# Optimization experiments

Hardware: AMD Instinct MI355X
Metric: run time of the kernel (lower is better)

Reference implementation:

```python
import jax, jax.numpy as jnp
import numpy as np

B, T, C = 4, 2048, 1024
N_HEAD = 16
HEAD_DIM = C // N_HEAD


def setup_inputs() -> dict:
    key = jax.random.key(0)
    k1, k2, k3 = jax.random.split(key, 3)
    x = jax.random.normal(k1, (B, T, C), dtype=jnp.float32)
    W_attn = jax.random.normal(k2, (C, 3 * C), dtype=jnp.float32) * (1.0 / np.sqrt(C))
    b_attn = jnp.zeros((3 * C,), dtype=jnp.float32)
    W_proj = jax.random.normal(k3, (C, C), dtype=jnp.float32) * (1.0 / np.sqrt(C))
    b_proj = jnp.zeros((C,), dtype=jnp.float32)
    return {"x": x, "W_attn": W_attn, "b_attn": b_attn, "W_proj": W_proj, "b_proj": b_proj}


def reference(x, W_attn, b_attn, W_proj, b_proj):
    Bx, Tx, Cx = x.shape
    qkv = x @ W_attn + b_attn  # (B,T,3C)
    q, k, v = jnp.split(qkv, 3, axis=-1)
    # (B, n_head, T, head_dim)
    def to_heads(t):
        return t.reshape(Bx, Tx, N_HEAD, HEAD_DIM).transpose(0, 2, 1, 3)
    q, k, v = to_heads(q), to_heads(k), to_heads(v)
    scale = 1.0 / np.sqrt(HEAD_DIM)
    scores = jnp.einsum('bhqd,bhkd->bhqk', q, k) * scale  # (B,H,T,T)
    causal = jnp.tril(jnp.ones((Tx, Tx), dtype=bool))
    scores = jnp.where(causal[None, None, :, :], scores, -jnp.inf)
    probs = jax.nn.softmax(scores, axis=-1)
    attn = jnp.einsum('bhqk,bhkd->bhqd', probs, v)  # (B,H,T,D)
    attn = attn.transpose(0, 2, 1, 3).reshape(Bx, Tx, Cx)
    return attn @ W_proj + b_proj
```

## Files before the change

kernel.cpp:

```cpp
#include <hip/hip_runtime.h>


typedef __attribute__((ext_vector_type(8))) __bf16 bf16x8;
typedef __attribute__((ext_vector_type(4))) float f32x4;
typedef __attribute__((ext_vector_type(4))) short s16x4;

__device__ __forceinline__ float bf2f(unsigned short h) {
    unsigned u = ((unsigned)h) << 16;
    return __builtin_bit_cast(float, u);
}
__device__ __forceinline__ unsigned short f2bf(float f) {
    unsigned u = __builtin_bit_cast(unsigned, f);
    u += 0x7fffu + ((u >> 16) & 1u);
    return (unsigned short)(u >> 16);
}
__device__ __forceinline__ unsigned pack2bf(float a, float b) {
    return (unsigned)f2bf(a) | ((unsigned)f2bf(b) << 16);
}
__device__ __forceinline__ void gload16(const unsigned short* g, unsigned short* l) {
    __builtin_amdgcn_global_load_lds(
        (const __attribute__((address_space(1))) unsigned int*)g,
        (__attribute__((address_space(3))) unsigned int*)l, 16, 0, 0);
}

__global__ void convert_kernel(const float* __restrict__ in, unsigned short* __restrict__ out,
                               long n) {
    long i = ((long)blockIdx.x * blockDim.x + threadIdx.x) * 4;
    if (i >= n) return;
    f32x4 v = *reinterpret_cast<const f32x4*>(&in[i]);
    s16x4 o;
    o[0] = (short)f2bf(v[0]);
    o[1] = (short)f2bf(v[1]);
    o[2] = (short)f2bf(v[2]);
    o[3] = (short)f2bf(v[3]);
    *reinterpret_cast<s16x4*>(&out[i]) = o;
}

__global__ void transpose_kernel(const float* __restrict__ W,
                                 unsigned short* __restrict__ Wt,
                                 int K, int N) {
    __shared__ float t[32][33];
    const int tid = threadIdx.x;
    const int n0 = blockIdx.x * 32, k0 = blockIdx.y * 32;
    const int row = tid >> 3, c4 = (tid & 7) * 4;
    f32x4 v = *reinterpret_cast<const f32x4*>(&W[(size_t)(k0 + row) * N + n0 + c4]);
    t[row][c4 + 0] = v[0];
    t[row][c4 + 1] = v[1];
    t[row][c4 + 2] = v[2];
    t[row][c4 + 3] = v[3];
    __syncthreads();
    s16x4 o;
    o[0] = (short)f2bf(t[c4 + 0][row]);
    o[1] = (short)f2bf(t[c4 + 1][row]);
    o[2] = (short)f2bf(t[c4 + 2][row]);
    o[3] = (short)f2bf(t[c4 + 3][row]);
    *reinterpret_cast<s16x4*>(&Wt[(size_t)(n0 + row) * K + k0 + c4]) = o;
}

template <int MODE>
__global__ __launch_bounds__(256, 2)
void gemm_kernel(const unsigned short* __restrict__ A,
                 const unsigned short* __restrict__ Bt,
                 const float* __restrict__ bias,
                 float* __restrict__ Cout,
                 unsigned short* __restrict__ Qo,
                 unsigned short* __restrict__ Ko,
                 unsigned short* __restrict__ Vto,
                 int M, int N, int Kd) {
    __shared__ unsigned short As[2][128 * 32];
    __shared__ unsigned short Bs[2][128 * 32];
    const int tid = threadIdx.x;
    const int wave = tid >> 6, lane = tid & 63;
    const int l15 = lane & 15, lhi = lane >> 4;
    const int wm = wave >> 1, wn = wave & 1;
    const int m0 = blockIdx.x * 128, n0 = blockIdx.y * 128;

    f32x4 acc[4][4];
#pragma unroll
    for (int i = 0; i < 4; i++)
#pragma unroll
        for (int j = 0; j < 4; j++) acc[i][j] = f32x4{0.f, 0.f, 0.f, 0.f};

    const int r0 = tid >> 2, cb = (tid & 3) * 8;
    const unsigned short* Ap = &A[(size_t)(m0 + r0) * Kd + cb];
    const unsigned short* Bp = &Bt[(size_t)(n0 + r0) * Kd + cb];
    const size_t K64 = (size_t)64 * Kd;

#define STAGE(buf, k0)                                      \
    do {                                                    \
        gload16(Ap + (k0), &As[buf][tid * 8]);              \
        gload16(Ap + K64 + (k0), &As[buf][64 * 32 + tid * 8]); \
        gload16(Bp + (k0), &Bs[buf][tid * 8]);              \
        gload16(Bp + K64 + (k0), &Bs[buf][64 * 32 + tid * 8]); \
    } while (0)

#define COMPUTE(buf)                                                                         \
    do {                                                                                     \
        bf16x8 af[4], bfr[4];                                                                \
        _Pragma("unroll") for (int i = 0; i < 4; i++) {                                      \
            af[i]  = *reinterpret_cast<const bf16x8*>(&As[buf][(wm * 64 + i * 16 + l15) * 32 + lhi * 8]); \
            bfr[i] = *reinterpret_cast<const bf16x8*>(&Bs[buf][(wn * 64 + i * 16 + l15) * 32 + lhi * 8]); \
        }                                                                                    \
        _Pragma("unroll") for (int i = 0; i < 4; i++)                                        \
            _Pragma("unroll") for (int j = 0; j < 4; j++)                                    \
                acc[i][j] = __builtin_amdgcn_mfma_f32_16x16x32_bf16(af[i], bfr[j], acc[i][j], 0, 0, 0); \
    } while (0)

    STAGE(0, 0);
    __syncthreads();
    for (int k0 = 0; k0 < Kd; k0 += 64) {
        STAGE(1, k0 + 32);
        COMPUTE(0);
        __syncthreads();
        if (k0 + 64 < Kd) STAGE(0, k0 + 64);
        COMPUTE(1);
        __syncthreads();
    }
#undef STAGE
#undef COMPUTE

#pragma unroll
    for (int j = 0; j < 4; j++) {
        const int col = n0 + wn * 64 + j * 16 + l15;
        const float bv = bias[col];
#pragma unroll
        for (int i = 0; i < 4; i++) {
            const int rbase = m0 + wm * 64 + i * 16 + lhi * 4;
#pragma unroll
            for (int r = 0; r < 4; r++) {
                const int row = rbase + r;
                const float oval = acc[i][j][r] + bv;
                if (MODE == 0) {
                    Cout[(size_t)row * N + col] = oval;
                } else {
                    const int sel = col >> 10, c1 = col & 1023;
                    const int h = c1 >> 6, d = c1 & 63;
                    const int b = row >> 11, t = row & 2047;
                    if (sel == 0)
                        Qo[(((size_t)(b * 16 + h)) * 2048 + t) * 64 + d] = f2bf(oval * 0.125f);
                    else if (sel == 1)
                        Ko[(((size_t)(b * 16 + h)) * 2048 + t) * 64 + d] = f2bf(oval);
                    else
                        Vto[(((size_t)(b * 16 + h)) * 64 + d) * 2048 + t] = f2bf(oval);
                }
            }
        }
    }
}

__global__ __launch_bounds__(256, 2)
void attn_kernel(const unsigned short* __restrict__ Q,
                 const unsigned short* __restrict__ Kg,
                 const unsigned short* __restrict__ Vt,
                 unsigned short* __restrict__ Aout) {
    __shared__ unsigned int Pl[4][16 * 36];
    const int tid = threadIdx.x, wave = tid >> 6, lane = tid & 63;
    const int l15 = lane & 15, lhi = lane >> 4;
    const int bid = blockIdx.x;
    const int head = bid & 63;
    const int j = bid >> 6;
    const int qb = (j < 4) ? j : (11 - j);
    const int q0w = qb * 256 + wave * 64;
    const unsigned short* Qh = Q + (size_t)head * (2048 * 64);
    const unsigned short* Kh = Kg + (size_t)head * (2048 * 64);
    const unsigned short* Vh = Vt + (size_t)head * (64 * 2048);
    unsigned int* P = &Pl[wave][0];

    bf16x8 qfr[4][2];
#pragma unroll
    for (int qf = 0; qf < 4; qf++)
#pragma unroll
        for (int dh = 0; dh < 2; dh++)
            qfr[qf][dh] = *reinterpret_cast<const bf16x8*>(
                &Qh[(size_t)(q0w + qf * 16 + l15) * 64 + dh * 32 + lhi * 8]);

    f32x4 o[4][4];
#pragma unroll
    for (int df = 0; df < 4; df++)
#pragma unroll
        for (int qf = 0; qf < 4; qf++) o[df][qf] = f32x4{0.f, 0.f, 0.f, 0.f};
    float m[4] = {-1e30f, -1e30f, -1e30f, -1e30f};
    float l[4] = {0.f, 0.f, 0.f, 0.f};

    const int ntiles = (q0w >> 6) + 1;
    for (int t = 0; t < ntiles; ++t) {
        const int kt = t * 64;
        const bool masked = (t == ntiles - 1);
        bf16x8 kfr[4][2], vfr[4][2];
#pragma unroll
        for (int kf = 0; kf < 4; kf++)
#pragma unroll
            for (int dh = 0; dh < 2; dh++)
                kfr[kf][dh] = *reinterpret_cast<const bf16x8*>(
                    &Kh[(size_t)(kt + kf * 16 + l15) * 64 + dh * 32 + lhi * 8]);
#pragma unroll
        for (int df = 0; df < 4; df++)
#pragma unroll
            for (int kc = 0; kc < 2; kc++)
                vfr[df][kc] = *reinterpret_cast<const bf16x8*>(
                    &Vh[(size_t)(df * 16 + l15) * 2048 + kt + kc * 32 + lhi * 8]);

#pragma unroll
        for (int qf = 0; qf < 4; qf++) {
            f32x4 s[4];
#pragma unroll
            for (int kf = 0; kf < 4; kf++) {
                s[kf] = __builtin_amdgcn_mfma_f32_16x16x32_bf16(kfr[kf][0], qfr[qf][0],
                                                                f32x4{0.f, 0.f, 0.f, 0.f}, 0, 0, 0);
                s[kf] = __builtin_amdgcn_mfma_f32_16x16x32_bf16(kfr[kf][1], qfr[qf][1], s[kf], 0, 0, 0);
            }
            if (masked) {
#pragma unroll
                for (int kf = 0; kf < 4; kf++)
#pragma unroll
                    for (int r = 0; r < 4; r++)
                        if (kf * 16 + lhi * 4 + r > qf * 16 + l15) s[kf][r] = -1e30f;
            }
            float tm = s[0][0];
#pragma unroll
            for (int kf = 0; kf < 4; kf++)
#pragma unroll
                for (int r = 0; r < 4; r++) tm = fmaxf(tm, s[kf][r]);
            tm = fmaxf(tm, __shfl_xor(tm, 16));
            tm = fmaxf(tm, __shfl_xor(tm, 32));
            const float mn = fmaxf(m[qf], tm);
            const float corr = __expf(m[qf] - mn);
            m[qf] = mn;
            float rs = 0.f;
#pragma unroll
            for (int kf = 0; kf < 4; kf++)
#pragma unroll
                for (int r = 0; r < 4; r++) {
                    const float p = __expf(s[kf][r] - mn);
                    s[kf][r] = p;
                    rs += p;
                }
            rs += __shfl_xor(rs, 16);
            rs += __shfl_xor(rs, 32);
            l[qf] = l[qf] * corr + rs;
#pragma unroll
            for (int df = 0; df < 4; df++)
#pragma unroll
                for (int r = 0; r < 4; r++) o[df][qf][r] *= corr;

#pragma unroll
            for (int kf = 0; kf < 4; kf++) {
                P[l15 * 36 + kf * 8 + lhi * 2 + 0] = pack2bf(s[kf][0], s[kf][1]);
                P[l15 * 36 + kf * 8 + lhi * 2 + 1] = pack2bf(s[kf][2], s[kf][3]);
            }
            asm volatile("s_waitcnt lgkmcnt(0)" ::: "memory");
            bf16x8 pb0 = *reinterpret_cast<const bf16x8*>(&P[l15 * 36 + 0 * 16 + lhi * 4]);
            bf16x8 pb1 = *reinterpret_cast<const bf16x8*>(&P[l15 * 36 + 1 * 16 + lhi * 4]);
#pragma unroll
            for (int df = 0; df < 4; df++) {
                o[df][qf] = __builtin_amdgcn_mfma_f32_16x16x32_bf16(vfr[df][0], pb0, o[df][qf], 0, 0, 0);
                o[df][qf] = __builtin_amdgcn_mfma_f32_16x16x32_bf16(vfr[df][1], pb1, o[df][qf], 0, 0, 0);
            }
        }
    }

    const int b = head >> 4, h = head & 15;
#pragma unroll
    for (int qf = 0; qf < 4; qf++) {
        const float inv = 1.0f / l[qf];
        unsigned short* op = Aout + ((size_t)(b * 2048 + q0w + qf * 16 + l15)) * 1024 + h * 64;
#pragma unroll
        for (int df = 0; df < 4; df++) {
            *reinterpret_cast<unsigned*>(&op[df * 16 + lhi * 4]) =
                pack2bf(o[df][qf][0] * inv, o[df][qf][1] * inv);
            *reinterpret_cast<unsigned*>(&op[df * 16 + lhi * 4 + 2]) =
                pack2bf(o[df][qf][2] * inv, o[df][qf][3] * inv);
        }
    }
}

extern "C" void kernel_launch(void* const* d_in, const int* in_sizes, int n_in,
                              void* d_out, int out_size, void* d_ws, size_t ws_size,
                              hipStream_t stream) {
    const float* x     = (const float*)d_in[0];
    const float* Wattn = (const float*)d_in[1];
    const float* battn = (const float*)d_in[2];
    const float* Wproj = (const float*)d_in[3];
    const float* bproj = (const float*)d_in[4];
    float* out = (float*)d_out;

    unsigned short* ws = (unsigned short*)d_ws;
    const size_t HS = (size_t)4 * 16 * 2048 * 64;
    unsigned short* Qb  = ws;
    unsigned short* Kb  = Qb + HS;
    unsigned short* Vtb = Kb + HS;
    unsigned short* Ab  = Vtb + HS;
    unsigned short* Wta = Ab + HS;
    unsigned short* Wtp = Wta + (size_t)3072 * 1024;
    unsigned short* xb  = Wtp + (size_t)1024 * 1024;

    convert_kernel<<<8192, 256, 0, stream>>>(x, xb, (long)HS);
    transpose_kernel<<<dim3(96, 32), 256, 0, stream>>>(Wattn, Wta, 1024, 3072);
    transpose_kernel<<<dim3(32, 32), 256, 0, stream>>>(Wproj, Wtp, 1024, 1024);
    gemm_kernel<1><<<dim3(64, 24), 256, 0, stream>>>(xb, Wta, battn, nullptr, Qb, Kb, Vtb,
                                                     8192, 3072, 1024);
    attn_kernel<<<512, 256, 0, stream>>>(Qb, Kb, Vtb, Ab);
    gemm_kernel<0><<<dim3(64, 8), 256, 0, stream>>>(Ab, Wtp, bproj, out, nullptr, nullptr, nullptr,
                                                    8192, 1024, 1024);
}
```

Baseline: 218.6 us.

## Add 256x256-tile QKV GEMM with swizzled LDS, deeper pipeline and XCD-aware block mapping

Replaces the 128x128 QKV projection GEMM with a dedicated 512-thread kernel using 256x256 output tiles. It uses an XOR-swizzled LDS layout, a multi-stage global_load_lds pipeline with explicit vmcnt waits and barriers, and s_setprio around the MFMA bursts. Block indices are remapped so neighbouring tiles land on the same XCD for better L2 reuse. The larger tiles raise arithmetic intensity and cut LDS bank conflicts, at the cost of one block per CU, much higher register and LDS use, and only 384 blocks.

```diff
diff --git a/kernel.cpp b/kernel.cpp
--- a/kernel.cpp
+++ b/kernel.cpp
@@ -5,10 +5,6 @@
 typedef __attribute__((ext_vector_type(4))) float f32x4;
 typedef __attribute__((ext_vector_type(4))) short s16x4;
 
-__device__ __forceinline__ float bf2f(unsigned short h) {
-    unsigned u = ((unsigned)h) << 16;
-    return __builtin_bit_cast(float, u);
-}
 __device__ __forceinline__ unsigned short f2bf(float f) {
     unsigned u = __builtin_bit_cast(unsigned, f);
     u += 0x7fffu + ((u >> 16) & 1u);
@@ -57,15 +53,124 @@
     *reinterpret_cast<s16x4*>(&Wt[(size_t)(n0 + row) * K + k0 + c4]) = o;
 }
 
-template <int MODE>
+__global__ __launch_bounds__(512, 1)
+void gemm256_kernel(const unsigned short* __restrict__ A,
+                    const unsigned short* __restrict__ Bt,
+                    const float* __restrict__ bias,
+                    unsigned short* __restrict__ Qo,
+                    unsigned short* __restrict__ Ko,
+                    unsigned short* __restrict__ Vto,
+                    int Kd) {
+    __shared__ unsigned short As[2][2][256 * 32];
+    __shared__ unsigned short Bs[2][2][256 * 32];
+    const int tid = threadIdx.x;
+    const int wave = tid >> 6, lane = tid & 63;
+    const int l15 = lane & 15, lhi = lane >> 4;
+    const int wm = wave >> 2, wn = wave & 3;
+    const int sw = (l15 & 8) << 2;
+    const int wg = (blockIdx.x & 7) * 48 + (blockIdx.x >> 3);
+    const int bm = wg / 12, bn = wg % 12;
+    const int m0 = bm * 256, n0 = bn * 256;
+
+    f32x4 acc[8][4];
+#pragma unroll
+    for (int i = 0; i < 8; i++)
+#pragma unroll
+        for (int j = 0; j < 4; j++) acc[i][j] = f32x4{0.f, 0.f, 0.f, 0.f};
+
+    const int L0 = tid * 16;
+    const int Ls0 = L0 ^ (((L0 >> 9) & 1) << 5);
+    const size_t ga0 = (size_t)(Ls0 >> 6) * Kd + ((Ls0 & 63) >> 1);
+    const size_t ga1 = ga0 + (size_t)128 * Kd;
+    const unsigned short* Ap = A + (size_t)m0 * Kd;
+    const unsigned short* Bp = Bt + (size_t)n0 * Kd;
+
+#define STAGEH(dst, src, kofs)                                                    \
+    do {                                                                          \
+        gload16((src) + ga0 + (kofs), (unsigned short*)((char*)(dst) + L0));      \
+        gload16((src) + ga1 + (kofs), (unsigned short*)((char*)(dst) + 8192 + L0)); \
+    } while (0)
+
+#define VWAIT2 asm volatile("s_waitcnt vmcnt(2)" ::: "memory")
+
+#define PHASE(db, ks, qm, STMT, WAITS)                                                     \
+    do {                                                                                   \
+        char* ab_ = (char*)&As[db][ks][0];                                                 \
+        char* bb_ = (char*)&Bs[db][ks][0];                                                 \
+        const int ar_ = (wm * 128 + (qm) * 64 + l15) * 64 + (lhi * 16 ^ sw);               \
+        const int br_ = (wn * 64 + l15) * 64 + (lhi * 16 ^ sw);                            \
+        bf16x8 av_[4], bv_[4];                                                             \
+        _Pragma("unroll") for (int t_ = 0; t_ < 4; t_++) {                                 \
+            av_[t_] = *(const bf16x8*)(ab_ + ar_ + t_ * 1024);                             \
+            bv_[t_] = *(const bf16x8*)(bb_ + br_ + t_ * 1024);                             \
+        }                                                                                  \
+        STMT;                                                                              \
+        WAITS;                                                                             \
+        __builtin_amdgcn_s_barrier();                                                      \
+        __builtin_amdgcn_s_setprio(1);                                                     \
+        _Pragma("unroll") for (int t_ = 0; t_ < 4; t_++)                                   \
+            _Pragma("unroll") for (int n_ = 0; n_ < 4; n_++)                               \
+                acc[(qm) * 4 + t_][n_] = __builtin_amdgcn_mfma_f32_16x16x32_bf16(          \
+                    av_[t_], bv_[n_], acc[(qm) * 4 + t_][n_], 0, 0, 0);                    \
+        __builtin_amdgcn_s_setprio(0);                                                     \
+        __builtin_amdgcn_s_barrier();                                                      \
+    } while (0)
+
+    STAGEH(&As[0][0][0], Ap, 0);
+    STAGEH(&Bs[0][0][0], Bp, 0);
+    STAGEH(&As[0][1][0], Ap, 32);
+    STAGEH(&Bs[0][1][0], Bp, 32);
+    STAGEH(&As[1][0][0], Ap, 64);
+    VWAIT2;
+    __builtin_amdgcn_s_barrier();
+
+    const int NITER = Kd >> 7;
+    for (int i = 0; i < NITER; ++i) {
+        const int kt1 = (2 * i + 1) * 64, kt2 = (2 * i + 2) * 64, kt3 = kt2 + 64;
+        const bool sg = (i < NITER - 1);
+        PHASE(0, 0, 0, { STAGEH(&Bs[1][0][0], Bp, kt1); }, );
+        PHASE(0, 1, 0, { STAGEH(&As[1][1][0], Ap, kt1 + 32); }, );
+        PHASE(0, 0, 1, { STAGEH(&Bs[1][1][0], Bp, kt1 + 32); }, );
+        PHASE(0, 1, 1, { if (sg) STAGEH(&As[0][0][0], Ap, kt2); }, VWAIT2);
+        PHASE(1, 0, 0, { if (sg) STAGEH(&Bs[0][0][0], Bp, kt2); }, );
+        PHASE(1, 1, 0, { if (sg) STAGEH(&As[0][1][0], Ap, kt2 + 32); }, );
+        PHASE(1, 0, 1, { if (sg) STAGEH(&Bs[0][1][0], Bp, kt2 + 32); }, );
+        PHASE(1, 1, 1, { if (sg) STAGEH(&As[1][0][0], Ap, kt3); }, VWAIT2);
+    }
+#undef PHASE
+#undef STAGEH
+#undef VWAIT2
+
+#pragma unroll
+    for (int nf = 0; nf < 4; nf++) {
+        const int col = n0 + wn * 64 + nf * 16 + l15;
+        const float bv = bias[col];
+        const int sel = col >> 10, c1 = col & 1023;
+        const int h = c1 >> 6, d = c1 & 63;
+#pragma unroll
+        for (int mf = 0; mf < 8; mf++) {
+            const int rbase = m0 + wm * 128 + mf * 16 + lhi * 4;
+#pragma unroll
+            for (int r = 0; r < 4; r++) {
+                const int row = rbase + r;
+                const float oval = acc[mf][nf][r] + bv;
+                const int b = row >> 11, t = row & 2047;
+                if (sel == 0)
+                    Qo[(((size_t)(b * 16 + h)) * 2048 + t) * 64 + d] = f2bf(oval * 0.125f);
+                else if (sel == 1)
+                    Ko[(((size_t)(b * 16 + h)) * 2048 + t) * 64 + d] = f2bf(oval);
+                else
+                    Vto[(((size_t)(b * 16 + h)) * 64 + d) * 2048 + t] = f2bf(oval);
+            }
+        }
+    }
+}
+
 __global__ __launch_bounds__(256, 2)
 void gemm_kernel(const unsigned short* __restrict__ A,
                  const unsigned short* __restrict__ Bt,
                  const float* __restrict__ bias,
                  float* __restrict__ Cout,
-                 unsigned short* __restrict__ Qo,
-                 unsigned short* __restrict__ Ko,
-                 unsigned short* __restrict__ Vto,
                  int M, int N, int Kd) {
     __shared__ unsigned short As[2][128 * 32];
     __shared__ unsigned short Bs[2][128 * 32];
@@ -86,11 +191,11 @@
     const unsigned short* Bp = &Bt[(size_t)(n0 + r0) * Kd + cb];
     const size_t K64 = (size_t)64 * Kd;
 
-#define STAGE(buf, k0)                                      \
-    do {                                                    \
-        gload16(Ap + (k0), &As[buf][tid * 8]);              \
+#define STAGE(buf, k0)                                         \
+    do {                                                       \
+        gload16(Ap + (k0), &As[buf][tid * 8]);                 \
         gload16(Ap + K64 + (k0), &As[buf][64 * 32 + tid * 8]); \
-        gload16(Bp + (k0), &Bs[buf][tid * 8]);              \
+        gload16(Bp + (k0), &Bs[buf][tid * 8]);                 \
         gload16(Bp + K64 + (k0), &Bs[buf][64 * 32 + tid * 8]); \
     } while (0)
 
@@ -127,23 +232,8 @@
         for (int i = 0; i < 4; i++) {
             const int rbase = m0 + wm * 64 + i * 16 + lhi * 4;
 #pragma unroll
-            for (int r = 0; r < 4; r++) {
-                const int row = rbase + r;
-                const float oval = acc[i][j][r] + bv;
-                if (MODE == 0) {
-                    Cout[(size_t)row * N + col] = oval;
-                } else {
-                    const int sel = col >> 10, c1 = col & 1023;
-                    const int h = c1 >> 6, d = c1 & 63;
-                    const int b = row >> 11, t = row & 2047;
-                    if (sel == 0)
-                        Qo[(((size_t)(b * 16 + h)) * 2048 + t) * 64 + d] = f2bf(oval * 0.125f);
-                    else if (sel == 1)
-                        Ko[(((size_t)(b * 16 + h)) * 2048 + t) * 64 + d] = f2bf(oval);
-                    else
-                        Vto[(((size_t)(b * 16 + h)) * 64 + d) * 2048 + t] = f2bf(oval);
-                }
-            }
+            for (int r = 0; r < 4; r++)
+                Cout[(size_t)(rbase + r) * N + col] = acc[i][j][r] + bv;
         }
     }
 }
@@ -297,9 +387,7 @@
     convert_kernel<<<8192, 256, 0, stream>>>(x, xb, (long)HS);
     transpose_kernel<<<dim3(96, 32), 256, 0, stream>>>(Wattn, Wta, 1024, 3072);
     transpose_kernel<<<dim3(32, 32), 256, 0, stream>>>(Wproj, Wtp, 1024, 1024);
-    gemm_kernel<1><<<dim3(64, 24), 256, 0, stream>>>(xb, Wta, battn, nullptr, Qb, Kb, Vtb,
-                                                     8192, 3072, 1024);
+    gemm256_kernel<<<384, 512, 0, stream>>>(xb, Wta, battn, Qb, Kb, Vtb, 1024);
     attn_kernel<<<512, 256, 0, stream>>>(Qb, Kb, Vtb, Ab);
-    gemm_kernel<0><<<dim3(64, 8), 256, 0, stream>>>(Ab, Wtp, bproj, out, nullptr, nullptr, nullptr,
-                                                    8192, 1024, 1024);
-}
+    gemm_kernel<<<dim3(64, 8), 256, 0, stream>>>(Ab, Wtp, bproj, out, 8192, 1024, 1024);
+}
```

Result: slower. 244.7 us (+11.9%).

## Deepen GEMM LDS pipeline to four stages with swizzled layout and manual waitcnt

Applied to the files above, without the earlier changes.

The GEMM mainloop moves from a double-buffered LDS scheme with __syncthreads to a four-slot ring that prefetches two k-steps ahead. It uses explicit vmcnt waits, raw s_barrier and s_setprio around the MFMA block. An XOR swizzle on the k-column offset is applied to both the global-to-LDS staging and the fragment reads, to cut LDS bank conflicts. This doubles LDS usage per block, which may reduce occupancy, and correctness now depends on hand-counted vmcnt values and on Kd being a multiple of 128.

```diff
diff --git a/kernel.cpp b/kernel.cpp
--- a/kernel.cpp
+++ b/kernel.cpp
@@ -5,10 +5,6 @@
 typedef __attribute__((ext_vector_type(4))) float f32x4;
 typedef __attribute__((ext_vector_type(4))) short s16x4;
 
-__device__ __forceinline__ float bf2f(unsigned short h) {
-    unsigned u = ((unsigned)h) << 16;
-    return __builtin_bit_cast(float, u);
-}
 __device__ __forceinline__ unsigned short f2bf(float f) {
     unsigned u = __builtin_bit_cast(unsigned, f);
     u += 0x7fffu + ((u >> 16) & 1u);
@@ -67,8 +63,8 @@
                  unsigned short* __restrict__ Ko,
                  unsigned short* __restrict__ Vto,
                  int M, int N, int Kd) {
-    __shared__ unsigned short As[2][128 * 32];
-    __shared__ unsigned short Bs[2][128 * 32];
+    __shared__ unsigned short As[4][128 * 32];
+    __shared__ unsigned short Bs[4][128 * 32];
     const int tid = threadIdx.x;
     const int wave = tid >> 6, lane = tid & 63;
     const int l15 = lane & 15, lhi = lane >> 4;
@@ -81,43 +77,66 @@
 #pragma unroll
         for (int j = 0; j < 4; j++) acc[i][j] = f32x4{0.f, 0.f, 0.f, 0.f};
 
-    const int r0 = tid >> 2, cb = (tid & 3) * 8;
-    const unsigned short* Ap = &A[(size_t)(m0 + r0) * Kd + cb];
-    const unsigned short* Bp = &Bt[(size_t)(n0 + r0) * Kd + cb];
+    const int r0 = tid >> 2;
+    const int cstage = (((tid & 3) ^ (r0 & 3)) << 3);
+    const unsigned short* Ap = &A[(size_t)(m0 + r0) * Kd + cstage];
+    const unsigned short* Bp = &Bt[(size_t)(n0 + r0) * Kd + cstage];
     const size_t K64 = (size_t)64 * Kd;
-
-#define STAGE(buf, k0)                                      \
-    do {                                                    \
-        gload16(Ap + (k0), &As[buf][tid * 8]);              \
-        gload16(Ap + K64 + (k0), &As[buf][64 * 32 + tid * 8]); \
-        gload16(Bp + (k0), &Bs[buf][tid * 8]);              \
-        gload16(Bp + K64 + (k0), &Bs[buf][64 * 32 + tid * 8]); \
+    const int csw = (lhi * 8) ^ ((l15 & 3) << 3);
+
+#define STAGE(sl, k0)                                   \
+    do {                                                \
+        gload16(Ap + (k0), &As[sl][tid * 8]);           \
+        gload16(Ap + K64 + (k0), &As[sl][2048 + tid * 8]); \
+        gload16(Bp + (k0), &Bs[sl][tid * 8]);           \
+        gload16(Bp + K64 + (k0), &Bs[sl][2048 + tid * 8]); \
     } while (0)
 
-#define COMPUTE(buf)                                                                         \
-    do {                                                                                     \
-        bf16x8 af[4], bfr[4];                                                                \
-        _Pragma("unroll") for (int i = 0; i < 4; i++) {                                      \
-            af[i]  = *reinterpret_cast<const bf16x8*>(&As[buf][(wm * 64 + i * 16 + l15) * 32 + lhi * 8]); \
-            bfr[i] = *reinterpret_cast<const bf16x8*>(&Bs[buf][(wn * 64 + i * 16 + l15) * 32 + lhi * 8]); \
-        }                                                                                    \
-        _Pragma("unroll") for (int i = 0; i < 4; i++)                                        \
-            _Pragma("unroll") for (int j = 0; j < 4; j++)                                    \
-                acc[i][j] = __builtin_amdgcn_mfma_f32_16x16x32_bf16(af[i], bfr[j], acc[i][j], 0, 0, 0); \
+#define VW4 asm volatile("s_waitcnt vmcnt(4)" ::: "memory")
+#define VW0 asm volatile("s_waitcnt vmcnt(0)" ::: "memory")
+
+#define PH(sl, sg, kc, WAITM)                                                              \
+    do {                                                                                   \
+        bf16x8 av_[4], bv_[4];                                                             \
+        _Pragma("unroll") for (int i_ = 0; i_ < 4; i_++) {                                 \
+            av_[i_] = *reinterpret_cast<const bf16x8*>(                                    \
+                &As[sl][(wm * 64 + i_ * 16 + l15) * 32 + csw]);                            \
+            bv_[i_] = *reinterpret_cast<const bf16x8*>(                                    \
+                &Bs[sl][(wn * 64 + i_ * 16 + l15) * 32 + csw]);                            \
+        }                                                                                  \
+        if (sg) STAGE((sl + 2) & 3, (kc) * 32);                                            \
+        WAITM;                                                                             \
+        __builtin_amdgcn_s_barrier();                                                      \
+        __builtin_amdgcn_s_setprio(1);                                                     \
+        _Pragma("unroll") for (int i_ = 0; i_ < 4; i_++)                                   \
+            _Pragma("unroll") for (int j_ = 0; j_ < 4; j_++)                               \
+                acc[i_][j_] = __builtin_amdgcn_mfma_f32_16x16x32_bf16(av_[i_], bv_[j_],    \
+                                                                      acc[i_][j_], 0, 0, 0); \
+        __builtin_amdgcn_s_setprio(0);                                                     \
+        __builtin_amdgcn_s_barrier();                                                      \
     } while (0)
 
     STAGE(0, 0);
-    __syncthreads();
-    for (int k0 = 0; k0 < Kd; k0 += 64) {
-        STAGE(1, k0 + 32);
-        COMPUTE(0);
-        __syncthreads();
-        if (k0 + 64 < Kd) STAGE(0, k0 + 64);
-        COMPUTE(1);
-        __syncthreads();
+    STAGE(1, 32);
+    VW4;
+    __builtin_amdgcn_s_barrier();
+
+    const int NPH = Kd >> 5;
+    for (int it = 0; it < (NPH >> 2) - 1; ++it) {
+        const int kc = it * 4;
+        PH(0, true, kc + 2, VW4);
+        PH(1, true, kc + 3, VW4);
+        PH(2, true, kc + 4, VW4);
+        PH(3, true, kc + 5, VW4);
     }
+    PH(0, true, NPH - 2, VW4);
+    PH(1, true, NPH - 1, VW4);
+    PH(2, false, 0, VW0);
+    PH(3, false, 0, VW0);
+#undef PH
 #undef STAGE
-#undef COMPUTE
+#undef VW4
+#undef VW0
 
 #pragma unroll
     for (int j = 0; j < 4; j++) {
```

New measurement: 216.1 us. No clear change (-1.1%).
